# Optimization experiments

Measured on AMD Instinct MI355X. Metric: run time of the kernel, lower is better.

## Reference

```python
import jax, jax.numpy as jnp
import numpy as np

NUM_HEADS = 16


def _local_attn(q, k, v, bias, nq, nk):
    """Blocked local attention, faithful to rearrange_to_dense_trunk semantics.
    q,k,v: [B,H,N,D]; bias: [B,Hb,N,N] (Hb broadcasts against H).
    Trunk i (queries [i*nq,(i+1)*nq)) attends keys at original indices
    [i*nq - pad_left, i*nq - pad_left + nk); out-of-range keys/values/bias are
    zero-padded (the module pads with zeros, no -inf key masking).
    Assumes N % nq == 0 (q_pad_length == 0, so the query mask loop is a no-op).
    """
    B, H, N, D = q.shape
    T = N // nq                      # n_trunks
    pad_left = (nk - nq) // 2
    Lp = (T - 1) * nq + nk           # padded key length so every window is full
    pad_right = Lp - pad_left - N
    k_p = jnp.pad(k, ((0, 0), (0, 0), (pad_left, pad_right), (0, 0)))
    v_p = jnp.pad(v, ((0, 0), (0, 0), (pad_left, pad_right), (0, 0)))
    b_p = jnp.pad(bias, ((0, 0), (0, 0), (0, 0), (pad_left, pad_right)))
    # window gather indices: [T, nk]
    kidx = jnp.arange(T)[:, None] * nq + jnp.arange(nk)[None, :]
    k_t = k_p[:, :, kidx, :]         # [B,H,T,nk,D]
    v_t = v_p[:, :, kidx, :]         # [B,H,T,nk,D]
    Bb, Hb = bias.shape[0], bias.shape[1]
    b_r = b_p.reshape(Bb, Hb, T, nq, Lp)
    b_t = jnp.take_along_axis(b_r, kidx[None, None, :, None, :], axis=-1)  # [Bb,Hb,T,nq,nk]
    q_t = q.reshape(B, H, T, nq, D)
    scores = jnp.einsum('bhtqd,bhtkd->bhtqk', q_t, k_t) + b_t
    w = jax.nn.softmax(scores, axis=-1)
    o = jnp.einsum('bhtqk,bhtkd->bhtqd', w, v_t)
    return o.reshape(B, H, N, D)


def setup_inputs() -> dict:
    key = jax.random.key(0)
    ks = jax.random.split(key, 8)
    B, N, C = 1, 4096, 256
    H, D = NUM_HEADS, 64
    HD = H * D
    q_x = jax.random.normal(ks[0], (B, N, C), dtype=jnp.float32)
    kv_x = jax.random.normal(ks[1], (B, N, C), dtype=jnp.float32)
    attn_bias = jax.random.normal(ks[2], (B, 1, N, N), dtype=jnp.float32) * 0.1
    Wq = jax.random.normal(ks[3], (C, HD), dtype=jnp.float32) / np.sqrt(C).astype(np.float32)
    Wk = jax.random.normal(ks[4], (C, HD), dtype=jnp.float32) / np.sqrt(C).astype(np.float32)
    Wv = jax.random.normal(ks[5], (C, HD), dtype=jnp.float32) / np.sqrt(C).astype(np.float32)
    Wg = jax.random.normal(ks[6], (C, HD), dtype=jnp.float32) / np.sqrt(C).astype(np.float32)
    Wo = jax.random.normal(ks[7], (HD, C), dtype=jnp.float32) / np.sqrt(HD).astype(np.float32)
    return {"q_x": q_x, "kv_x": kv_x, "attn_bias": attn_bias,
            "Wq": Wq, "Wk": Wk, "Wv": Wv, "Wg": Wg, "Wo": Wo,
            "n_queries": 64, "n_keys": 256}


def reference(q_x, kv_x, attn_bias, Wq, Wk, Wv, Wg, Wo, n_queries, n_keys):
    B, N, C = q_x.shape
    H = NUM_HEADS
    D = Wq.shape[-1] // H
    def split_heads(x):
        return x.reshape(B, N, H, D).transpose(0, 2, 1, 3)  # [B,H,N,D]
    q = split_heads(q_x @ Wq) / jnp.sqrt(jnp.float32(D))
    k = split_heads(kv_x @ Wk)
    v = split_heads(kv_x @ Wv)
    o = _local_attn(q, k, v, attn_bias, n_queries, n_keys)
    o = o.transpose(0, 2, 1, 3).reshape(B, N, H * D)
    g = jax.nn.sigmoid(q_x @ Wg)  # gating head
    return (o * g) @ Wo
```

## Files before the change

kernel.cpp:

```cpp
#include <hip/hip_runtime.h>

#define N_ 4096
#define C_ 256
#define H_ 16
#define D_ 64
#define HD_ 1024

typedef __attribute__((ext_vector_type(8))) __bf16 bf16x8;
typedef __attribute__((ext_vector_type(4))) __bf16 bf16x4;
typedef __attribute__((ext_vector_type(8))) _Float16 f16x8;
typedef __attribute__((ext_vector_type(4))) _Float16 f16x4;
typedef __attribute__((ext_vector_type(4))) float f32x4;

__device__ __forceinline__ void gload16(const void* g, void* l) {
    __builtin_amdgcn_global_load_lds(
        (const __attribute__((address_space(1))) unsigned int*)g,
        (__attribute__((address_space(3))) unsigned int*)l, 16, 0, 0);
}

struct bf2 { __bf16 h, l; };
__device__ __forceinline__ bf2 split_bf16(float v) {
    bf2 r;
    r.h = (__bf16)v;
    r.l = (__bf16)(v - (float)r.h);
    return r;
}

__global__ __launch_bounds__(256) void convert_kernel(
    const float* __restrict__ q_x, const float* __restrict__ kv_x,
    const float* __restrict__ Wq, const float* __restrict__ Wk,
    const float* __restrict__ Wv, const float* __restrict__ Wg,
    const float* __restrict__ Wo,
    _Float16* __restrict__ Xf, _Float16* __restrict__ WTf,
    __bf16* __restrict__ WoTh, __bf16* __restrict__ WoTl)
{
    __shared__ float ts[64][65];
    const int b = blockIdx.x;
    const int tid = threadIdx.x;

    if (b < 512) {
        const int seg = b >> 8;
        const float* src = seg ? kv_x : q_x;
        _Float16* df = Xf + (size_t)seg * 1048576;
        const int base = (b & 255) * 4096 + tid * 16;
#pragma unroll
        for (int q = 0; q < 4; ++q) {
            float4 v = *(const float4*)&src[base + q * 4];
            f16x4 fv;
            fv[0] = (_Float16)v.x; fv[1] = (_Float16)v.y;
            fv[2] = (_Float16)v.z; fv[3] = (_Float16)v.w;
            *(f16x4*)&df[base + q * 4] = fv;
        }
        return;
    }

    if (b < 768) {
        const int widx = (b - 512) >> 6;
        const int tile = (b - 512) & 63;
        const float* src = (widx == 0) ? Wq : (widx == 1) ? Wk : (widx == 2) ? Wv : Wg;
        _Float16* df = WTf + (size_t)widx * 262144;
        const int r0 = (tile >> 4) * 64;
        const int c0 = (tile & 15) * 64;
        {
            const int r = tid >> 2;
            const int cch = (tid & 3) * 16;
#pragma unroll
            for (int q = 0; q < 4; ++q) {
                float4 v = *(const float4*)&src[(size_t)(r0 + r) * 1024 + c0 + cch + q * 4];
                ts[r][cch + q * 4 + 0] = v.x;
                ts[r][cch + q * 4 + 1] = v.y;
                ts[r][cch + q * 4 + 2] = v.z;
                ts[r][cch + q * 4 + 3] = v.w;
            }
        }
        __syncthreads();
        {
            const int c = tid >> 2;
            const int rch = (tid & 3) * 16;
#pragma unroll
            for (int q = 0; q < 4; ++q) {
                f16x4 fv;
#pragma unroll
                for (int j = 0; j < 4; ++j)
                    fv[j] = (_Float16)ts[rch + q * 4 + j][c];
                *(f16x4*)&df[(size_t)(c0 + c) * 256 + r0 + rch + q * 4] = fv;
            }
        }
        return;
    }

    {
        const int tile = b - 768;
        const int r0 = (tile >> 2) * 64;
        const int c0 = (tile & 3) * 64;
        {
            const int r = tid >> 2;
            const int cch = (tid & 3) * 16;
#pragma unroll
            for (int q = 0; q < 4; ++q) {
                float4 v = *(const float4*)&Wo[(size_t)(r0 + r) * 256 + c0 + cch + q * 4];
                ts[r][cch + q * 4 + 0] = v.x;
                ts[r][cch + q * 4 + 1] = v.y;
                ts[r][cch + q * 4 + 2] = v.z;
                ts[r][cch + q * 4 + 3] = v.w;
            }
        }
        __syncthreads();
        {
            const int c = tid >> 2;
            const int rch = (tid & 3) * 16;
#pragma unroll
            for (int q = 0; q < 4; ++q) {
                bf16x4 hv, lv;
#pragma unroll
                for (int j = 0; j < 4; ++j) {
                    bf2 s = split_bf16(ts[rch + q * 4 + j][c]);
                    hv[j] = s.h; lv[j] = s.l;
                }
                *(bf16x4*)&WoTh[(size_t)(c0 + c) * 1024 + r0 + rch + q * 4] = hv;
                *(bf16x4*)&WoTl[(size_t)(c0 + c) * 1024 + r0 + rch + q * 4] = lv;
            }
        }
    }
}

__global__ __launch_bounds__(256) void proj_mfma(
    const _Float16* __restrict__ Xf, const _Float16* __restrict__ WTf,
    _Float16* __restrict__ qh, _Float16* __restrict__ kh,
    _Float16* __restrict__ vh, _Float16* __restrict__ gh)
{
    __shared__ __align__(16) _Float16 smem[2 * 8192];
    _Float16* As = smem;
    _Float16* Bs = smem + 8192;

    const int lb  = blockIdx.x;
    const int xcd = lb & 7;
    const int gr  = (lb >> 6) * 8 + xcd;
    const int g   = gr >> 5;
    const int m0  = (gr & 31) * 128;
    const int c0  = ((lb >> 3) & 7) * 128;

    const _Float16* A = Xf + ((g == 1 || g == 2) ? 1048576 : 0);
    const _Float16* B = WTf + (size_t)g * 262144;

    const int tid  = threadIdx.x;
    const int wave = tid >> 6;
    const int lane = tid & 63;
    const int wr   = wave >> 1;
    const int wc   = wave & 1;
    const int frow = lane & 15;
    const int grp  = lane >> 4;

    f32x4 acc[4][4];
#pragma unroll
    for (int i = 0; i < 4; ++i)
#pragma unroll
        for (int j = 0; j < 4; ++j) acc[i][j] = (f32x4){0.f, 0.f, 0.f, 0.f};

    const int srow = tid >> 3;
    const int sch  = tid & 7;

    for (int kt = 0; kt < 256; kt += 64) {
        __syncthreads();
#pragma unroll
        for (int p = 0; p < 4; ++p) {
            const int row = p * 32 + srow;
            const int koff = kt + ((sch ^ (row & 7)) << 3);
            gload16(A + (size_t)(m0 + row) * 256 + koff, (char*)As + p * 4096 + tid * 16);
            gload16(B + (size_t)(c0 + row) * 256 + koff, (char*)Bs + p * 4096 + tid * 16);
        }
        __syncthreads();

#pragma unroll
        for (int ks = 0; ks < 2; ++ks) {
            f16x8 af[4], bf[4];
#pragma unroll
            for (int f = 0; f < 4; ++f) {
                const int ra = wr * 64 + f * 16 + frow;
                const int rb = wc * 64 + f * 16 + frow;
                af[f] = *(const f16x8*)((char*)As + ra * 128 + (((ks * 4 + grp) ^ (ra & 7)) << 4));
                bf[f] = *(const f16x8*)((char*)Bs + rb * 128 + (((ks * 4 + grp) ^ (rb & 7)) << 4));
            }
#pragma unroll
            for (int i = 0; i < 4; ++i)
#pragma unroll
                for (int j = 0; j < 4; ++j)
                    acc[i][j] = __builtin_amdgcn_mfma_f32_16x16x32_f16(af[i], bf[j], acc[i][j], 0, 0, 0);
        }
    }

    const int rbase = grp * 4;
    if (g == 3) {
#pragma unroll
        for (int i = 0; i < 4; ++i)
#pragma unroll
            for (int j = 0; j < 4; ++j) {
                const int c = c0 + wc * 64 + j * 16 + frow;
#pragma unroll
                for (int v = 0; v < 4; ++v) {
                    const int n = m0 + wr * 64 + i * 16 + rbase + v;
                    gh[(size_t)n * HD_ + c] = (_Float16)(1.f / (1.f + __expf(-acc[i][j][v])));
                }
            }
    } else {
        const float scale = (g == 0) ? 0.125f : 1.f;
        _Float16* dst = (g == 0) ? qh : (g == 1) ? kh : vh;
#pragma unroll
        for (int i = 0; i < 4; ++i)
#pragma unroll
            for (int j = 0; j < 4; ++j) {
                const int c = c0 + wc * 64 + j * 16 + frow;
                const int hh = c >> 6, dd = c & 63;
#pragma unroll
                for (int v = 0; v < 4; ++v) {
                    const int n = m0 + wr * 64 + i * 16 + rbase + v;
                    dst[((size_t)hh * N_ + n) * D_ + dd] = (_Float16)(acc[i][j][v] * scale);
                }
            }
    }
}

__global__ __launch_bounds__(256) void attn_mfma(
    const _Float16* __restrict__ qh, const _Float16* __restrict__ kh,
    const _Float16* __restrict__ vh, const float* __restrict__ bias,
    const _Float16* __restrict__ gh,
    __bf16* __restrict__ o_hi, __bf16* __restrict__ o_lo)
{
    __shared__ __align__(16) char smem[59392];
    _Float16* Qs = (_Float16*)smem;
    char* Ks = smem + 8192;
    _Float16* Vs = (_Float16*)(smem + 8192);
    _Float16* Ps = (_Float16*)(smem + 25600);

    const int lb  = blockIdx.x;
    const int xcd = lb & 7;
    const int j_  = lb >> 3;
    const int h   = j_ >> 3;
    const int t   = xcd * 8 + (j_ & 7);
    const int tid = threadIdx.x;
    const int lane = tid & 63;
    const int wv = tid >> 6;
    const int frow = lane & 15;
    const int grp = lane >> 4;
    const int kbase = t * 64 - 96;

    const char* qbase = (const char*)qh + (size_t)(h * N_ + t * 64) * 128;
    const char* kbase_p = (const char*)kh + (size_t)h * N_ * 128;

#pragma unroll
    for (int q = 0; q < 2; ++q) {
        const int lin = q * 4096 + tid * 16;
        const int row = lin >> 7;
        const int ch = (lin >> 4) & 7;
        gload16(qbase + row * 128 + ((ch ^ (row & 7)) << 4), (char*)Qs + lin);
    }

    f32x4 sacc[16];

#pragma unroll
    for (int p = 0; p < 2; ++p) {
#pragma unroll
        for (int q = 0; q < 4; ++q) {
            const int lin = q * 4096 + tid * 16;
            const int row = lin >> 7;
            const int ch = (lin >> 4) & 7;
            const int kg = kbase + p * 128 + row;
            if ((unsigned)kg < (unsigned)N_) {
                gload16(kbase_p + (size_t)kg * 128 + ((ch ^ (row & 7)) << 4), Ks + lin);
            } else {
                *(float4*)(Ks + lin) = make_float4(0.f, 0.f, 0.f, 0.f);
            }
        }
        {
            const int rowg = t * 64 + wv * 16 + grp * 4;
#pragma unroll
            for (int j = 0; j < 8; ++j) {
                const int colg = kbase + p * 128 + j * 16 + frow;
                const bool ok = (unsigned)colg < (unsigned)N_;
#pragma unroll
                for (int v = 0; v < 4; ++v)
                    sacc[p * 8 + j][v] = ok ? bias[(size_t)(rowg + v) * N_ + colg] : 0.f;
            }
        }
        __syncthreads();
        const int rq = wv * 16 + frow;
#pragma unroll
        for (int ks = 0; ks < 2; ++ks) {
            const f16x8 aq = *(const f16x8*)((char*)Qs + rq * 128 + (((ks * 4 + grp) ^ (rq & 7)) << 4));
#pragma unroll
            for (int j = 0; j < 8; ++j) {
                const int rk = j * 16 + frow;
                const f16x8 bk = *(const f16x8*)(Ks + rk * 128 + (((ks * 4 + grp) ^ (rk & 7)) << 4));
                sacc[p * 8 + j] = __builtin_amdgcn_mfma_f32_16x16x32_f16(aq, bk, sacc[p * 8 + j], 0, 0, 0);
            }
        }
        __syncthreads();
    }

    float inv[4];
#pragma unroll
    for (int v = 0; v < 4; ++v) {
        float m = sacc[0][v];
#pragma unroll
        for (int f = 1; f < 16; ++f) m = fmaxf(m, sacc[f][v]);
        m = fmaxf(m, __shfl_xor(m, 1));
        m = fmaxf(m, __shfl_xor(m, 2));
        m = fmaxf(m, __shfl_xor(m, 4));
        m = fmaxf(m, __shfl_xor(m, 8));
        float l = 0.f;
#pragma unroll
        for (int f = 0; f < 16; ++f) {
            float e = __expf(sacc[f][v] - m);
            sacc[f][v] = e;
            l += e;
        }
        l += __shfl_xor(l, 1);
        l += __shfl_xor(l, 2);
        l += __shfl_xor(l, 4);
        l += __shfl_xor(l, 8);
        inv[v] = 1.f / l;
    }

    {
        const int rb = wv * 16 + grp * 4;
#pragma unroll
        for (int f = 0; f < 16; ++f) {
            const int col = (f >> 3) * 128 + (f & 7) * 16 + frow;
#pragma unroll
            for (int v = 0; v < 4; ++v)
                Ps[(rb + v) * 264 + col] = (_Float16)sacc[f][v];
        }
    }

    f32x4 oacc[4];
#pragma unroll
    for (int jd = 0; jd < 4; ++jd) oacc[jd] = (f32x4){0.f, 0.f, 0.f, 0.f};

#pragma unroll
    for (int c = 0; c < 2; ++c) {
        {
            const int sl = tid >> 1;
            const int d0 = (tid & 1) * 32;
            const int kg = kbase + c * 128 + sl;
            f16x8 vv[4];
            if ((unsigned)kg < (unsigned)N_) {
                const f16x8* vp = (const f16x8*)(vh + ((size_t)h * N_ + kg) * D_ + d0);
#pragma unroll
                for (int q = 0; q < 4; ++q) vv[q] = vp[q];
            } else {
#pragma unroll
                for (int q = 0; q < 4; ++q)
#pragma unroll
                    for (int e = 0; e < 8; ++e) vv[q][e] = (_Float16)0.f;
            }
#pragma unroll
            for (int q = 0; q < 4; ++q)
#pragma unroll
                for (int e = 0; e < 8; ++e)
                    Vs[(d0 + q * 8 + e) * 136 + sl] = vv[q][e];
        }
        __syncthreads();
        const int rp = wv * 16 + frow;
#pragma unroll
        for (int ks = 0; ks < 4; ++ks) {
            const f16x8 ap = *(const f16x8*)((char*)Ps + rp * 528 + c * 256 + ks * 64 + grp * 16);
#pragma unroll
            for (int jd = 0; jd < 4; ++jd) {
                const f16x8 bv = *(const f16x8*)((char*)Vs + (jd * 16 + frow) * 272 + ks * 64 + grp * 16);
                oacc[jd] = __builtin_amdgcn_mfma_f32_16x16x32_f16(ap, bv, oacc[jd], 0, 0, 0);
            }
        }
        __syncthreads();
    }

#pragma unroll
    for (int jd = 0; jd < 4; ++jd) {
        const int dcol = jd * 16 + frow;
        const int cg = h * 64 + dcol;
#pragma unroll
        for (int v = 0; v < 4; ++v) {
            const int n = t * 64 + wv * 16 + grp * 4 + v;
            const float gt = (float)gh[(size_t)n * HD_ + cg];
            const float val = oacc[jd][v] * inv[v] * gt;
            bf2 s = split_bf16(val);
            o_hi[(size_t)n * HD_ + cg] = s.h;
            o_lo[(size_t)n * HD_ + cg] = s.l;
        }
    }
}

__global__ __launch_bounds__(256) void out_mfma(
    const __bf16* __restrict__ o_hi, const __bf16* __restrict__ o_lo,
    const __bf16* __restrict__ WoTh, const __bf16* __restrict__ WoTl,
    float* __restrict__ out)
{
    __shared__ __align__(16) __bf16 smem[4 * 2048];
    __bf16* As_h = smem;
    __bf16* As_l = smem + 2048;
    __bf16* Bs_h = smem + 4096;
    __bf16* Bs_l = smem + 6144;

    const int lb  = blockIdx.x;
    const int xcd = lb & 7;
    const int idx = lb >> 3;
    const int rowg = (idx >> 2) * 8 + xcd;
    const int m0  = rowg * 64;
    const int c0  = (idx & 3) * 64;

    const int tid  = threadIdx.x;
    const int wave = tid >> 6;
    const int lane = tid & 63;
    const int wr   = wave >> 1;
    const int wc   = wave & 1;

    const int srow  = tid >> 2;
    const int selem = (tid & 3) * 8;
    const int sbyte = tid * 16;

    f32x4 acc[2][2];
#pragma unroll
    for (int i = 0; i < 2; ++i)
#pragma unroll
        for (int j = 0; j < 2; ++j) acc[i][j] = (f32x4){0.f, 0.f, 0.f, 0.f};

    const int frow = lane & 15;
    const int fk   = (lane >> 4) * 8;

    for (int kt = 0; kt < 1024; kt += 32) {
        __syncthreads();
        gload16(o_hi + (size_t)(m0 + srow) * HD_ + kt + selem, (char*)As_h + sbyte);
        gload16(o_lo + (size_t)(m0 + srow) * HD_ + kt + selem, (char*)As_l + sbyte);
        gload16(WoTh + (size_t)(c0 + srow) * HD_ + kt + selem, (char*)Bs_h + sbyte);
        gload16(WoTl + (size_t)(c0 + srow) * HD_ + kt + selem, (char*)Bs_l + sbyte);
        __syncthreads();

        bf16x8 afh[2], afl[2], bfh[2], bfl[2];
#pragma unroll
        for (int f = 0; f < 2; ++f) {
            const int ar = (wr * 32 + f * 16 + frow) * 32 + fk;
            const int br = (wc * 32 + f * 16 + frow) * 32 + fk;
            afh[f] = *(const bf16x8*)&As_h[ar];
            afl[f] = *(const bf16x8*)&As_l[ar];
            bfh[f] = *(const bf16x8*)&Bs_h[br];
            bfl[f] = *(const bf16x8*)&Bs_l[br];
        }
#pragma unroll
        for (int i = 0; i < 2; ++i)
#pragma unroll
            for (int j = 0; j < 2; ++j) {
                acc[i][j] = __builtin_amdgcn_mfma_f32_16x16x32_bf16(afh[i], bfh[j], acc[i][j], 0, 0, 0);
                acc[i][j] = __builtin_amdgcn_mfma_f32_16x16x32_bf16(afl[i], bfh[j], acc[i][j], 0, 0, 0);
                acc[i][j] = __builtin_amdgcn_mfma_f32_16x16x32_bf16(afh[i], bfl[j], acc[i][j], 0, 0, 0);
            }
    }

    const int rbase = (lane >> 4) * 4;
    const int colc  = lane & 15;
#pragma unroll
    for (int i = 0; i < 2; ++i)
#pragma unroll
        for (int j = 0; j < 2; ++j) {
            const int c = c0 + wc * 32 + j * 16 + colc;
#pragma unroll
            for (int v = 0; v < 4; ++v) {
                const int n = m0 + wr * 32 + i * 16 + rbase + v;
                out[(size_t)n * C_ + c] = acc[i][j][v];
            }
        }
}

extern "C" void kernel_launch(void* const* d_in, const int* in_sizes, int n_in,
                              void* d_out, int out_size, void* d_ws, size_t ws_size,
                              hipStream_t stream)
{
    const float* q_x  = (const float*)d_in[0];
    const float* kv_x = (const float*)d_in[1];
    const float* bias = (const float*)d_in[2];
    const float* Wq   = (const float*)d_in[3];
    const float* Wk   = (const float*)d_in[4];
    const float* Wv   = (const float*)d_in[5];
    const float* Wg   = (const float*)d_in[6];
    const float* Wo   = (const float*)d_in[7];
    float* out = (float*)d_out;

    char* ws = (char*)d_ws;
    const size_t MB = 1048576;
    _Float16* qh  = (_Float16*)(ws);
    _Float16* kh  = (_Float16*)(ws + 8  * MB);
    _Float16* vh  = (_Float16*)(ws + 16 * MB);
    _Float16* gh  = (_Float16*)(ws + 24 * MB);
    __bf16* o_hi  = (__bf16*)(ws + 32 * MB);
    __bf16* o_lo  = (__bf16*)(ws + 40 * MB);
    _Float16* Xf  = (_Float16*)(ws + 48 * MB);
    _Float16* WTf = (_Float16*)(ws + 52 * MB);
    __bf16* WoTh  = (__bf16*)(ws + 54 * MB);
    __bf16* WoTl  = (__bf16*)(ws + 54 * MB + 524288);

    convert_kernel<<<832, 256, 0, stream>>>(q_x, kv_x, Wq, Wk, Wv, Wg, Wo,
                                            Xf, WTf, WoTh, WoTl);
    proj_mfma<<<1024, 256, 0, stream>>>(Xf, WTf, qh, kh, vh, gh);
    attn_mfma<<<1024, 256, 0, stream>>>(qh, kh, vh, bias, gh, o_hi, o_lo);
    out_mfma<<<256, 256, 0, stream>>>(o_hi, o_lo, WoTh, WoTl, out);
}
```

Baseline: 173.3 us.

## Stage epilogues through LDS for vectorized stores and widen out-proj K tile with swizzle

The projection kernel now writes its results into a padded LDS tile, then issues 16-byte vector stores to q/k/v/g. The attention epilogue stages normalized outputs in LDS so each thread reads the gate vector-wise and writes 16-byte bf16 hi/lo chunks. The output GEMM doubles its K step to 64 with an XOR-swizzled LDS layout, which halves the barrier count and reduces bank conflicts. The cost is extra barriers, LDS round trips and larger shared memory usage, which may reduce occupancy.

```diff
diff --git a/kernel.cpp b/kernel.cpp
--- a/kernel.cpp
+++ b/kernel.cpp
@@ -129,9 +129,9 @@
     _Float16* __restrict__ qh, _Float16* __restrict__ kh,
     _Float16* __restrict__ vh, _Float16* __restrict__ gh)
 {
-    __shared__ __align__(16) _Float16 smem[2 * 8192];
-    _Float16* As = smem;
-    _Float16* Bs = smem + 8192;
+    __shared__ __align__(16) char psmem[34816];
+    _Float16* As = (_Float16*)psmem;
+    _Float16* Bs = (_Float16*)(psmem + 16384);
 
     const int lb  = blockIdx.x;
     const int xcd = lb & 7;
@@ -189,34 +189,41 @@
         }
     }
 
-    const int rbase = grp * 4;
-    if (g == 3) {
+    __syncthreads();
+    _Float16* Epi = (_Float16*)psmem;
+    {
+        const float scale = (g == 0) ? 0.125f : 1.f;
 #pragma unroll
         for (int i = 0; i < 4; ++i)
 #pragma unroll
             for (int j = 0; j < 4; ++j) {
-                const int c = c0 + wc * 64 + j * 16 + frow;
+                const int rr = wr * 64 + i * 16 + grp * 4;
+                const int cc = wc * 64 + j * 16 + frow;
 #pragma unroll
                 for (int v = 0; v < 4; ++v) {
-                    const int n = m0 + wr * 64 + i * 16 + rbase + v;
-                    gh[(size_t)n * HD_ + c] = (_Float16)(1.f / (1.f + __expf(-acc[i][j][v])));
+                    float x = acc[i][j][v];
+                    x = (g == 3) ? 1.f / (1.f + __expf(-x)) : x * scale;
+                    Epi[(rr + v) * 136 + cc] = (_Float16)x;
                 }
             }
-    } else {
-        const float scale = (g == 0) ? 0.125f : 1.f;
-        _Float16* dst = (g == 0) ? qh : (g == 1) ? kh : vh;
-#pragma unroll
-        for (int i = 0; i < 4; ++i)
-#pragma unroll
-            for (int j = 0; j < 4; ++j) {
-                const int c = c0 + wc * 64 + j * 16 + frow;
-                const int hh = c >> 6, dd = c & 63;
-#pragma unroll
-                for (int v = 0; v < 4; ++v) {
-                    const int n = m0 + wr * 64 + i * 16 + rbase + v;
-                    dst[((size_t)hh * N_ + n) * D_ + dd] = (_Float16)(acc[i][j][v] * scale);
-                }
-            }
+    }
+    __syncthreads();
+    {
+        const int ch   = tid & 15;
+        const int head = ch >> 3;
+        const int e8   = (ch & 7) * 8;
+#pragma unroll
+        for (int p = 0; p < 8; ++p) {
+            const int r = p * 16 + (tid >> 4);
+            const f16x8 val = *(const f16x8*)&Epi[r * 136 + head * 64 + e8];
+            if (g == 3) {
+                *(f16x8*)&gh[(size_t)(m0 + r) * HD_ + c0 + head * 64 + e8] = val;
+            } else {
+                _Float16* dst = (g == 0) ? qh : (g == 1) ? kh : vh;
+                const int hh = (c0 >> 6) + head;
+                *(f16x8*)&dst[((size_t)hh * N_ + m0 + r) * D_ + e8] = val;
+            }
+        }
     }
 }
 
@@ -231,6 +238,7 @@
     char* Ks = smem + 8192;
     _Float16* Vs = (_Float16*)(smem + 8192);
     _Float16* Ps = (_Float16*)(smem + 25600);
+    float* Oe = (float*)(smem + 25600);
 
     const int lb  = blockIdx.x;
     const int xcd = lb & 7;
@@ -376,16 +384,45 @@
 #pragma unroll
     for (int jd = 0; jd < 4; ++jd) {
         const int dcol = jd * 16 + frow;
-        const int cg = h * 64 + dcol;
 #pragma unroll
         for (int v = 0; v < 4; ++v) {
-            const int n = t * 64 + wv * 16 + grp * 4 + v;
-            const float gt = (float)gh[(size_t)n * HD_ + cg];
-            const float val = oacc[jd][v] * inv[v] * gt;
-            bf2 s = split_bf16(val);
-            o_hi[(size_t)n * HD_ + cg] = s.h;
-            o_lo[(size_t)n * HD_ + cg] = s.l;
-        }
+            const int rn = wv * 16 + grp * 4 + v;
+            Oe[rn * 68 + dcol] = oacc[jd][v] * inv[v];
+        }
+    }
+    __syncthreads();
+    {
+        const int r   = tid >> 2;
+        const int seg = tid & 3;
+        const int n   = t * 64 + r;
+        const int cg0 = h * 64 + seg * 16;
+        const float* orow = &Oe[r * 68 + seg * 16];
+        f32x4 o0 = *(const f32x4*)&orow[0];
+        f32x4 o1 = *(const f32x4*)&orow[4];
+        f32x4 o2 = *(const f32x4*)&orow[8];
+        f32x4 o3 = *(const f32x4*)&orow[12];
+        const f16x8 g0 = *(const f16x8*)&gh[(size_t)n * HD_ + cg0];
+        const f16x8 g1 = *(const f16x8*)&gh[(size_t)n * HD_ + cg0 + 8];
+        float vals[16];
+#pragma unroll
+        for (int e = 0; e < 4; ++e) {
+            vals[e]      = o0[e] * (float)g0[e];
+            vals[4 + e]  = o1[e] * (float)g0[4 + e];
+            vals[8 + e]  = o2[e] * (float)g1[e];
+            vals[12 + e] = o3[e] * (float)g1[4 + e];
+        }
+        bf16x8 hi0, hi1, lo0, lo1;
+#pragma unroll
+        for (int e = 0; e < 8; ++e) {
+            bf2 s0 = split_bf16(vals[e]);
+            bf2 s1 = split_bf16(vals[8 + e]);
+            hi0[e] = s0.h; lo0[e] = s0.l;
+            hi1[e] = s1.h; lo1[e] = s1.l;
+        }
+        *(bf16x8*)&o_hi[(size_t)n * HD_ + cg0]     = hi0;
+        *(bf16x8*)&o_hi[(size_t)n * HD_ + cg0 + 8] = hi1;
+        *(bf16x8*)&o_lo[(size_t)n * HD_ + cg0]     = lo0;
+        *(bf16x8*)&o_lo[(size_t)n * HD_ + cg0 + 8] = lo1;
     }
 }
 
@@ -394,11 +431,11 @@
     const __bf16* __restrict__ WoTh, const __bf16* __restrict__ WoTl,
     float* __restrict__ out)
 {
-    __shared__ __align__(16) __bf16 smem[4 * 2048];
+    __shared__ __align__(16) __bf16 smem[4 * 4096];
     __bf16* As_h = smem;
-    __bf16* As_l = smem + 2048;
-    __bf16* Bs_h = smem + 4096;
-    __bf16* Bs_l = smem + 6144;
+    __bf16* As_l = smem + 4096;
+    __bf16* Bs_h = smem + 8192;
+    __bf16* Bs_l = smem + 12288;
 
     const int lb  = blockIdx.x;
     const int xcd = lb & 7;
@@ -412,10 +449,8 @@
     const int lane = tid & 63;
     const int wr   = wave >> 1;
     const int wc   = wave & 1;
-
-    const int srow  = tid >> 2;
-    const int selem = (tid & 3) * 8;
-    const int sbyte = tid * 16;
+    const int frow = lane & 15;
+    const int grp  = lane >> 4;
 
     f32x4 acc[2][2];
 #pragma unroll
@@ -423,44 +458,52 @@
 #pragma unroll
         for (int j = 0; j < 2; ++j) acc[i][j] = (f32x4){0.f, 0.f, 0.f, 0.f};
 
-    const int frow = lane & 15;
-    const int fk   = (lane >> 4) * 8;
-
-    for (int kt = 0; kt < 1024; kt += 32) {
-        __syncthreads();
-        gload16(o_hi + (size_t)(m0 + srow) * HD_ + kt + selem, (char*)As_h + sbyte);
-        gload16(o_lo + (size_t)(m0 + srow) * HD_ + kt + selem, (char*)As_l + sbyte);
-        gload16(WoTh + (size_t)(c0 + srow) * HD_ + kt + selem, (char*)Bs_h + sbyte);
-        gload16(WoTl + (size_t)(c0 + srow) * HD_ + kt + selem, (char*)Bs_l + sbyte);
-        __syncthreads();
-
-        bf16x8 afh[2], afl[2], bfh[2], bfl[2];
-#pragma unroll
-        for (int f = 0; f < 2; ++f) {
-            const int ar = (wr * 32 + f * 16 + frow) * 32 + fk;
-            const int br = (wc * 32 + f * 16 + frow) * 32 + fk;
-            afh[f] = *(const bf16x8*)&As_h[ar];
-            afl[f] = *(const bf16x8*)&As_l[ar];
-            bfh[f] = *(const bf16x8*)&Bs_h[br];
-            bfl[f] = *(const bf16x8*)&Bs_l[br];
-        }
-#pragma unroll
-        for (int i = 0; i < 2; ++i)
-#pragma unroll
-            for (int j = 0; j < 2; ++j) {
-                acc[i][j] = __builtin_amdgcn_mfma_f32_16x16x32_bf16(afh[i], bfh[j], acc[i][j], 0, 0, 0);
-                acc[i][j] = __builtin_amdgcn_mfma_f32_16x16x32_bf16(afl[i], bfh[j], acc[i][j], 0, 0, 0);
-                acc[i][j] = __builtin_amdgcn_mfma_f32_16x16x32_bf16(afh[i], bfl[j], acc[i][j], 0, 0, 0);
-            }
-    }
-
-    const int rbase = (lane >> 4) * 4;
-    const int colc  = lane & 15;
+    for (int kt = 0; kt < 1024; kt += 64) {
+        __syncthreads();
+#pragma unroll
+        for (int p = 0; p < 2; ++p) {
+            const int lin = p * 4096 + tid * 16;
+            const int row = lin >> 7;
+            const int ch  = (lin >> 4) & 7;
+            const int koff = kt + ((ch ^ (row & 7)) << 3);
+            gload16(o_hi + (size_t)(m0 + row) * HD_ + koff, (char*)As_h + lin);
+            gload16(o_lo + (size_t)(m0 + row) * HD_ + koff, (char*)As_l + lin);
+            gload16(WoTh + (size_t)(c0 + row) * HD_ + koff, (char*)Bs_h + lin);
+            gload16(WoTl + (size_t)(c0 + row) * HD_ + koff, (char*)Bs_l + lin);
+        }
+        __syncthreads();
+
+#pragma unroll
+        for (int ks = 0; ks < 2; ++ks) {
+            bf16x8 afh[2], afl[2], bfh[2], bfl[2];
+#pragma unroll
+            for (int f = 0; f < 2; ++f) {
+                const int ra = wr * 32 + f * 16 + frow;
+                const int rb = wc * 32 + f * 16 + frow;
+                const int ca = ((ks * 4 + grp) ^ (ra & 7)) << 4;
+                const int cb = ((ks * 4 + grp) ^ (rb & 7)) << 4;
+                afh[f] = *(const bf16x8*)((char*)As_h + ra * 128 + ca);
+                afl[f] = *(const bf16x8*)((char*)As_l + ra * 128 + ca);
+                bfh[f] = *(const bf16x8*)((char*)Bs_h + rb * 128 + cb);
+                bfl[f] = *(const bf16x8*)((char*)Bs_l + rb * 128 + cb);
+            }
+#pragma unroll
+            for (int i = 0; i < 2; ++i)
+#pragma unroll
+                for (int j = 0; j < 2; ++j) {
+                    acc[i][j] = __builtin_amdgcn_mfma_f32_16x16x32_bf16(afh[i], bfh[j], acc[i][j], 0, 0, 0);
+                    acc[i][j] = __builtin_amdgcn_mfma_f32_16x16x32_bf16(afl[i], bfh[j], acc[i][j], 0, 0, 0);
+                    acc[i][j] = __builtin_amdgcn_mfma_f32_16x16x32_bf16(afh[i], bfl[j], acc[i][j], 0, 0, 0);
+                }
+        }
+    }
+
+    const int rbase = grp * 4;
 #pragma unroll
     for (int i = 0; i < 2; ++i)
 #pragma unroll
         for (int j = 0; j < 2; ++j) {
-            const int c = c0 + wc * 32 + j * 16 + colc;
+            const int c = c0 + wc * 32 + j * 16 + frow;
 #pragma unroll
             for (int v = 0; v < 4; ++v) {
                 const int n = m0 + wr * 32 + i * 16 + rbase + v;
```

Result: no change. 173.4 us (+0.0%).
